# Performance work log

Measured on AMD Instinct MI355X. Metric: run time of the kernel, lower is better.

## Reference

```python
import jax, jax.numpy as jnp
import numpy as np

NUM_HEADS = 8
HEAD_DIM = 64
INPUT_DIM = 512
OUT_DIM = 512
INNER_DIM = NUM_HEADS * HEAD_DIM


def setup_inputs() -> dict:
    key = jax.random.key(0)
    ks = jax.random.split(key, 5)
    B, T = 4, 2048
    x = jax.random.normal(ks[0], (B, T, INPUT_DIM), dtype=jnp.float32)
    Wk = jax.random.normal(ks[1], (INNER_DIM, INPUT_DIM), dtype=jnp.float32)
    Wq = jax.random.normal(ks[2], (INNER_DIM, INPUT_DIM), dtype=jnp.float32)
    Wv = jax.random.normal(ks[3], (INNER_DIM, INPUT_DIM), dtype=jnp.float32)
    Wp = jax.random.normal(ks[4], (OUT_DIM, INNER_DIM), dtype=jnp.float32)
    return {"x": x, "Wk": Wk, "Wq": Wq, "Wv": Wv, "Wp": Wp, "causal_mask": 0}


def reference(x, Wk, Wq, Wv, Wp, causal_mask):
    B, T, C = x.shape
    c_scale = C ** (-0.5)

    def proj(W):
        # (B,T,C) @ (C,inner) -> (B,T,H,D) -> (B,H,T,D), scaled by C^-0.5
        return (jnp.einsum('btc,ic->bti', x, W)
                .reshape(B, T, NUM_HEADS, HEAD_DIM)
                .transpose(0, 2, 1, 3) * c_scale)

    q, k, v = proj(Wq), proj(Wk), proj(Wv)
    # scores: (B,H,T,T), scaled by head_dim^-0.5
    weight = jnp.einsum('bhqd,bhkd->bhqk', q, k) * (HEAD_DIM ** (-0.5))
    if causal_mask:
        mask = jnp.triu(jnp.ones((T, T), dtype=bool), k=1)
        weight = jnp.where(mask, -jnp.inf, weight)
    weight = jax.nn.softmax(weight, axis=-1)
    out = jnp.einsum('bhqk,bhkd->bhqd', weight, v)  # (B,H,T,D)
    out = out.transpose(0, 2, 1, 3).reshape(B, T, INNER_DIM)
    # final projection scaled by inner_dim^-0.5 (projection.size(-1))
    out = jnp.einsum('bti,oi->bto', out, Wp) * (INNER_DIM ** (-0.5))
    return out
```

## Files before the change

### kernel.cpp

```cpp
#include <hip/hip_runtime.h>
#include <stdint.h>

#define T_SEQ 2048
#define NB 4
#define NH 8
#define DH 64
#define CD 512

typedef __attribute__((ext_vector_type(8))) short bf16x8;
typedef __attribute__((ext_vector_type(4))) uint16_t u16x4;
typedef __attribute__((ext_vector_type(4))) float f32x4;
typedef __attribute__((ext_vector_type(16))) float f32x16;
typedef __attribute__((ext_vector_type(4))) int i32x4;

#if __has_builtin(__builtin_amdgcn_exp2f)
#define EXP2(x) __builtin_amdgcn_exp2f(x)
#else
#define EXP2(x) exp2f(x)
#endif

__device__ __forceinline__ uint16_t f2bf(float f) {
  uint32_t u = __float_as_uint(f);
  u += 0x7FFFu + ((u >> 16) & 1u);
  return (uint16_t)(u >> 16);
}

__device__ __forceinline__ uint32_t cvtpk_bf16(float lo, float hi) {
  uint32_t r;
  asm("v_cvt_pk_bf16_f32 %0, %1, %2" : "=v"(r) : "v"(lo), "v"(hi));
  return r;
}

__device__ __forceinline__ void gload_lds16(const void* g, void* l) {
  __builtin_amdgcn_global_load_lds((const __attribute__((address_space(1))) void*)g,
                                   (__attribute__((address_space(3))) void*)l, 16, 0, 0);
}

__global__ __launch_bounds__(256) void cvt_all(const float* __restrict__ x,
    const float* __restrict__ wq, const float* __restrict__ wk,
    const float* __restrict__ wv, const float* __restrict__ wp,
    uint16_t* __restrict__ ws) {
  int i = blockIdx.x * 256 + threadIdx.x;
  int e = i * 4;
  const float* src;
  uint16_t* dst;
  if (e < 4194304) {
    src = x + e; dst = ws + e;
  } else {
    int r = e - 4194304;
    int w = r >> 18;
    int o = r & 262143;
    const float* W = (w == 0) ? wq : (w == 1) ? wk : (w == 2) ? wv : wp;
    src = W + o;
    dst = ws + 4194304 + (w << 18) + o;
  }
  float4 v = *(const float4*)src;
  u16x4 o4 = { f2bf(v.x), f2bf(v.y), f2bf(v.z), f2bf(v.w) };
  *(u16x4*)dst = o4;
}

__device__ __forceinline__ void gemm_bt_tile(const uint16_t* __restrict__ A,
                                             const uint16_t* __restrict__ Bt,
                                             int m0, int n0,
                                             uint16_t* As, uint16_t* Bs,
                                             f32x4 acc[4][4]) {
  const int tid = threadIdx.x;
  const int lane = tid & 63;
  const int wave = tid >> 6;
  const int wr = (wave >> 1) * 64, wc = (wave & 1) * 64;
  const int l15 = lane & 15, l4 = lane >> 4;

#pragma unroll
  for (int m = 0; m < 4; ++m)
#pragma unroll
    for (int n = 0; n < 4; ++n)
      acc[m][n] = (f32x4){0.f, 0.f, 0.f, 0.f};

  for (int kt = 0; kt < 8; ++kt) {
#pragma unroll
    for (int is = 0; is < 4; ++is) {
      int p = is * 4096 + tid * 16;
      int g = p ^ (((p >> 7) & 7) << 4);
      int row = g >> 7, colb = g & 127;
      gload_lds16((const char*)A + (size_t)(m0 + row) * 1024 + kt * 128 + colb,
                  (char*)As + p);
      gload_lds16((const char*)Bt + (size_t)(n0 + row) * 1024 + kt * 128 + colb,
                  (char*)Bs + p);
    }
    __syncthreads();
#pragma unroll
    for (int ks = 0; ks < 2; ++ks) {
      bf16x8 af[4], bfr[4];
#pragma unroll
      for (int m = 0; m < 4; ++m) {
        int row = wr + m * 16 + l15;
        int byt = (row * 128 + ks * 64 + l4 * 16) ^ ((row & 7) << 4);
        af[m] = *(const bf16x8*)((const char*)As + byt);
      }
#pragma unroll
      for (int n = 0; n < 4; ++n) {
        int row = wc + n * 16 + l15;
        int byt = (row * 128 + ks * 64 + l4 * 16) ^ ((row & 7) << 4);
        bfr[n] = *(const bf16x8*)((const char*)Bs + byt);
      }
#pragma unroll
      for (int m = 0; m < 4; ++m)
#pragma unroll
        for (int n = 0; n < 4; ++n)
          acc[m][n] = __builtin_amdgcn_mfma_f32_16x16x32_bf16(af[m], bfr[n], acc[m][n], 0, 0, 0);
    }
    __syncthreads();
  }
}

__global__ __launch_bounds__(256) void proj_kernel(const uint16_t* __restrict__ xb,
    const uint16_t* __restrict__ wbase, uint16_t* __restrict__ qkv,
    float qscale, float kvscale) {
  __shared__ __align__(16) uint16_t As[128 * 64];
  __shared__ __align__(16) uint16_t Bs[128 * 64];
  int z = blockIdx.z;
  const uint16_t* W = wbase + (size_t)z * 262144;
  uint16_t* outb = qkv + (size_t)z * 4194304;
  float scale = (z == 0) ? qscale : kvscale;
  f32x4 acc[4][4];
  int lane = threadIdx.x & 63, wave = threadIdx.x >> 6;
  int wr = (wave >> 1) * 64, wc = (wave & 1) * 64;
  int l15 = lane & 15, l4 = lane >> 4;

  if (z < 2) {
    int m0 = blockIdx.x * 128, n0 = blockIdx.y * 128;
    gemm_bt_tile(xb, W, m0, n0, As, Bs, acc);
#pragma unroll
    for (int m = 0; m < 4; ++m)
#pragma unroll
      for (int n = 0; n < 4; ++n)
#pragma unroll
        for (int j = 0; j < 4; ++j) {
          int row = m0 + wr + m * 16 + l4 * 4 + j;
          int col = n0 + wc + n * 16 + l15;
          int b = row >> 11, t = row & 2047;
          int h = col >> 6, d = col & 63;
          outb[((size_t)(b * NH + h) * T_SEQ + t) * DH + d] = f2bf(acc[m][n][j] * scale);
        }
  } else {
    int m0 = blockIdx.y * 128, n0 = blockIdx.x * 128;
    gemm_bt_tile(W, xb, m0, n0, As, Bs, acc);
#pragma unroll
    for (int m = 0; m < 4; ++m)
#pragma unroll
      for (int n = 0; n < 4; ++n)
#pragma unroll
        for (int j = 0; j < 4; ++j) {
          int row = m0 + wr + m * 16 + l4 * 4 + j;
          int col = n0 + wc + n * 16 + l15;
          int h = row >> 6, d = row & 63;
          int b = col >> 11, t = col & 2047;
          outb[((size_t)(b * NH + h) * DH + d) * T_SEQ + t] = f2bf(acc[m][n][j] * scale);
        }
  }
}

__global__ __launch_bounds__(512, 4) void attn5(const uint16_t* __restrict__ Q,
    const uint16_t* __restrict__ K, const uint16_t* __restrict__ VT,
    uint16_t* __restrict__ AO) {
  __shared__ __align__(16) char smem[65536];

  int bid = blockIdx.x;
  int swz = (bid & 7) * 64 + (bid >> 3);
  int qt = swz & 15, bh = swz >> 4;
  int b = bh >> 3, h = bh & 7;
  int tid = threadIdx.x, lane = tid & 63, wave = tid >> 6;
  int l31 = lane & 31, hi = lane >> 5;
  int p = tid >> 8;
  int tin = tid & 255;
  int w4 = wave & 3;

  const char* Kb  = (const char*)(K  + (size_t)bh * T_SEQ * DH) + (size_t)p * 131072;
  const char* VTb = (const char*)(VT + (size_t)bh * DH * T_SEQ);
  const uint16_t* Qrow = Q + ((size_t)bh * T_SEQ + qt * 128 + w4 * 32 + l31) * DH;
  char* pbase = smem + p * 32768;

  auto stage = [&](int t) {
    char* kd = pbase + (t & 1) * 8192;
    char* vd = pbase + 16384 + (t & 1) * 8192;
    const char* ksrc = Kb + (size_t)t * 8192;
#pragma unroll
    for (int c = 0; c < 2; ++c) {
      int pp = c * 4096 + tin * 16;
      int g = pp ^ (((pp >> 7) & 7) << 4);
      gload_lds16(ksrc + g, kd + pp);
      int row = g >> 7, off = g & 127;
      gload_lds16(VTb + (size_t)row * 4096 + p * 2048 + (size_t)t * 128 + off, vd + pp);
    }
  };

  bf16x8 qf[4];
#pragma unroll
  for (int m = 0; m < 4; ++m)
    qf[m] = *(const bf16x8*)((const char*)Qrow + m * 32 + hi * 16);

  f32x16 Oacc[2];
#pragma unroll
  for (int dB = 0; dB < 2; ++dB) Oacc[dB] = (f32x16)(0.f);
  float lp0 = 0.f, lp1 = 0.f, lp2 = 0.f, lp3 = 0.f;

  stage(0);

  for (int kt = 0; kt < 16; ++kt) {
    if (kt + 1 < 16) stage(kt + 1);
    if (kt + 1 < 16) asm volatile("s_waitcnt vmcnt(4)\n\ts_barrier" ::: "memory");
    else             asm volatile("s_waitcnt vmcnt(0)\n\ts_barrier" ::: "memory");

    const char* Kc = pbase + (kt & 1) * 8192;
    const char* Vc = pbase + 16384 + (kt & 1) * 8192;

    f32x16 s0 = (f32x16)(0.f), s1 = (f32x16)(0.f);
    __builtin_amdgcn_s_setprio(1);
#pragma unroll
    for (int m = 0; m < 4; ++m) {
      int row0 = l31;
      int byt0 = (row0 * 128 + m * 32 + hi * 16) ^ ((row0 & 7) << 4);
      bf16x8 kf0 = *(const bf16x8*)(Kc + byt0);
      s0 = __builtin_amdgcn_mfma_f32_32x32x16_bf16(kf0, qf[m], s0, 0, 0, 0);
      int row1 = 32 + l31;
      int byt1 = (row1 * 128 + m * 32 + hi * 16) ^ ((row1 & 7) << 4);
      bf16x8 kf1 = *(const bf16x8*)(Kc + byt1);
      s1 = __builtin_amdgcn_mfma_f32_32x32x16_bf16(kf1, qf[m], s1, 0, 0, 0);
    }
    __builtin_amdgcn_s_setprio(0);

    uint32_t pa_[2][4], pb_[2][4];
    {
      float e0[16], e1[16];
#pragma unroll
      for (int r = 0; r < 16; ++r) e0[r] = EXP2(s0[r]);
#pragma unroll
      for (int r = 0; r < 16; ++r) e1[r] = EXP2(s1[r]);
#pragma unroll
      for (int r = 0; r < 16; ++r) {
        if ((r & 3) == 0)      { lp0 += e0[r]; lp0 += e1[r]; }
        else if ((r & 3) == 1) { lp1 += e0[r]; lp1 += e1[r]; }
        else if ((r & 3) == 2) { lp2 += e0[r]; lp2 += e1[r]; }
        else                   { lp3 += e0[r]; lp3 += e1[r]; }
      }
#pragma unroll
      for (int g = 0; g < 4; ++g) {
        pa_[0][g] = cvtpk_bf16(e0[4 * g], e0[4 * g + 1]);
        pb_[0][g] = cvtpk_bf16(e0[4 * g + 2], e0[4 * g + 3]);
        pa_[1][g] = cvtpk_bf16(e1[4 * g], e1[4 * g + 1]);
        pb_[1][g] = cvtpk_bf16(e1[4 * g + 2], e1[4 * g + 3]);
      }
    }

#pragma unroll
    for (int km = 0; km < 4; ++km) {
      const int Tt = km >> 1;
      const int g0 = (km & 1) * 2;
      uint32_t w0 = pa_[Tt][g0], w2 = pa_[Tt][g0 + 1];
      uint32_t w1 = pb_[Tt][g0], w3 = pb_[Tt][g0 + 1];
      asm volatile("v_permlane32_swap_b32 %0, %1" : "+v"(w0), "+v"(w2));
      asm volatile("v_permlane32_swap_b32 %0, %1" : "+v"(w1), "+v"(w3));
      i32x4 pw = { (int)w0, (int)w1, (int)w2, (int)w3 };
      bf16x8 paf = __builtin_bit_cast(bf16x8, pw);
      __builtin_amdgcn_s_setprio(1);
#pragma unroll
      for (int dB = 0; dB < 2; ++dB) {
        int row = dB * 32 + l31;
        int byt = (row * 128 + km * 32 + hi * 16) ^ ((row & 7) << 4);
        bf16x8 vf = *(const bf16x8*)(Vc + byt);
        Oacc[dB] = __builtin_amdgcn_mfma_f32_32x32x16_bf16(paf, vf, Oacc[dB], 0, 0, 0);
      }
      __builtin_amdgcn_s_setprio(0);
    }

    asm volatile("s_waitcnt lgkmcnt(0)\n\ts_barrier" ::: "memory");
  }

  float lpart = (lp0 + lp1) + (lp2 + lp3);
  float lsum = lpart + __shfl_xor(lpart, 32, 64);
  float* cm = (float*)smem;
  float* slot = cm + (size_t)w4 * 2112 + lane * 33;
  if (p == 1) {
#pragma unroll
    for (int dB = 0; dB < 2; ++dB)
#pragma unroll
      for (int r = 0; r < 16; ++r)
        slot[dB * 16 + r] = Oacc[dB][r];
    slot[32] = lsum;
  }
  __syncthreads();
  if (p == 0) {
    float inv = 1.f / (lsum + slot[32]);
    f32x16 o0, o1;
#pragma unroll
    for (int r = 0; r < 16; ++r) {
      o0[r] = Oacc[0][r] + slot[r];
      o1[r] = Oacc[1][r] + slot[16 + r];
    }
    int qb0 = qt * 128 + w4 * 32;
#pragma unroll
    for (int r = 0; r < 16; ++r) {
      int qoff = (r & 3) + 8 * (r >> 2) + 4 * hi;
      float invr = __shfl(inv, qoff, 64);
      int t = qb0 + qoff;
      size_t base = ((size_t)(b * T_SEQ + t)) * 512 + h * 64;
      AO[base + l31]      = f2bf(o0[r] * invr);
      AO[base + 32 + l31] = f2bf(o1[r] * invr);
    }
  }
}

__global__ __launch_bounds__(256) void final_kernel(const uint16_t* __restrict__ ab,
    const uint16_t* __restrict__ wpb, float* __restrict__ out, float scale) {
  __shared__ __align__(16) uint16_t As[128 * 64];
  __shared__ __align__(16) uint16_t Bs[128 * 64];
  int m0 = blockIdx.x * 128, n0 = blockIdx.y * 128;
  f32x4 acc[4][4];
  gemm_bt_tile(ab, wpb, m0, n0, As, Bs, acc);
  int lane = threadIdx.x & 63, wave = threadIdx.x >> 6;
  int wr = (wave >> 1) * 64, wc = (wave & 1) * 64;
  int l15 = lane & 15, l4 = lane >> 4;
#pragma unroll
  for (int m = 0; m < 4; ++m)
#pragma unroll
    for (int n = 0; n < 4; ++n)
#pragma unroll
      for (int j = 0; j < 4; ++j) {
        int row = m0 + wr + m * 16 + l4 * 4 + j;
        int col = n0 + wc + n * 16 + l15;
        out[(size_t)row * 512 + col] = acc[m][n][j] * scale;
      }
}

extern "C" void kernel_launch(void* const* d_in, const int* in_sizes, int n_in,
                              void* d_out, int out_size, void* d_ws, size_t ws_size,
                              hipStream_t stream) {
  const float* x  = (const float*)d_in[0];
  const float* Wk = (const float*)d_in[1];
  const float* Wq = (const float*)d_in[2];
  const float* Wv = (const float*)d_in[3];
  const float* Wp = (const float*)d_in[4];
  uint16_t* ws = (uint16_t*)d_ws;

  uint16_t* xb  = ws;
  uint16_t* wqb = ws + 4194304;
  uint16_t* qkv = ws + 4194304 + 4 * 262144;
  uint16_t* qb  = qkv;
  uint16_t* kb  = qkv + 4194304;
  uint16_t* vtb = qkv + 2 * 4194304;
  uint16_t* ao  = xb;
  uint16_t* wpb = wqb + 3 * 262144;

  const float c_scale = 0.04419417382415922f;
  const float qscale = c_scale * 0.125f * 1.4426950408889634f;
  const float fscale = c_scale;

  cvt_all<<<dim3(5120), dim3(256), 0, stream>>>(x, Wq, Wk, Wv, Wp, ws);
  proj_kernel<<<dim3(64, 4, 3), dim3(256), 0, stream>>>(xb, wqb, qkv, qscale, c_scale);
  attn5<<<dim3(512), dim3(512), 0, stream>>>(qb, kb, vtb, ao);
  final_kernel<<<dim3(64, 4), dim3(256), 0, stream>>>(ao, wpb, (float*)d_out, fscale);
}
```

Baseline: 91.25 us.

## Split attention over four key ranges with a separate combine kernel

Adds an attention kernel that divides the key sequence into four chunks. Each of 2048 smaller blocks computes unnormalized partial outputs and row sums for one chunk, and a new combine kernel adds the partials, normalizes them and writes the head-interleaved layout. This raises the number of independent blocks, and the V operand is now read straight from global memory instead of being staged in LDS. In exchange it writes and re-reads bf16 partial outputs through workspace, adds a kernel launch, and only takes this path when the workspace is large enough.

```diff
diff --git a/kernel.cpp b/kernel.cpp
--- a/kernel.cpp
+++ b/kernel.cpp
@@ -8,6 +8,7 @@
 #define CD 512
 
 typedef __attribute__((ext_vector_type(8))) short bf16x8;
+typedef __attribute__((ext_vector_type(8))) uint16_t u16x8;
 typedef __attribute__((ext_vector_type(4))) uint16_t u16x4;
 typedef __attribute__((ext_vector_type(4))) float f32x4;
 typedef __attribute__((ext_vector_type(16))) float f32x16;
@@ -23,6 +24,10 @@
   uint32_t u = __float_as_uint(f);
   u += 0x7FFFu + ((u >> 16) & 1u);
   return (uint16_t)(u >> 16);
+}
+
+__device__ __forceinline__ float bf2f(uint16_t u) {
+  return __uint_as_float(((uint32_t)u) << 16);
 }
 
 __device__ __forceinline__ uint32_t cvtpk_bf16(float lo, float hi) {
@@ -160,6 +165,143 @@
   }
 }
 
+__global__ __launch_bounds__(256) void attn6(const uint16_t* __restrict__ Q,
+    const uint16_t* __restrict__ K, const uint16_t* __restrict__ VT,
+    uint16_t* __restrict__ Op, float* __restrict__ Lp) {
+  __shared__ __align__(16) char kbuf[2][8192];
+
+  int bid = blockIdx.x;
+  int swz = (bid & 7) * 256 + (bid >> 3);
+  int qt = swz & 15, qtr = (swz >> 4) & 3, bh = swz >> 6;
+  int tid = threadIdx.x, lane = tid & 63, wave = tid >> 6;
+  int l31 = lane & 31, hi = lane >> 5;
+
+  const char* Kb = (const char*)(K + (size_t)bh * T_SEQ * DH) + (size_t)qtr * 65536;
+  const char* Vb = (const char*)(VT + (size_t)bh * DH * T_SEQ) + (size_t)qtr * 1024
+                   + (size_t)l31 * 4096 + (size_t)hi * 16;
+  const uint16_t* Qrow = Q + ((size_t)bh * T_SEQ + qt * 128 + wave * 32 + l31) * DH;
+
+  auto stage = [&](int t) {
+    char* kd = &kbuf[t & 1][0];
+    const char* ksrc = Kb + (size_t)t * 8192;
+#pragma unroll
+    for (int c = 0; c < 2; ++c) {
+      int pp = c * 4096 + tid * 16;
+      int g = pp ^ (((pp >> 7) & 7) << 4);
+      gload_lds16(ksrc + g, kd + pp);
+    }
+  };
+
+  bf16x8 qf[4];
+#pragma unroll
+  for (int m = 0; m < 4; ++m)
+    qf[m] = *(const bf16x8*)((const char*)Qrow + m * 32 + hi * 16);
+
+  f32x16 Oacc[2];
+  Oacc[0] = (f32x16)(0.f);
+  Oacc[1] = (f32x16)(0.f);
+  float lp0 = 0.f, lp1 = 0.f, lp2 = 0.f, lp3 = 0.f;
+
+  stage(0);
+  asm volatile("s_waitcnt vmcnt(0)\n\ts_barrier" ::: "memory");
+
+  for (int kt = 0; kt < 8; ++kt) {
+    if (kt + 1 < 8) stage(kt + 1);
+    const char* Kc = &kbuf[kt & 1][0];
+
+    f32x16 s0 = (f32x16)(0.f), s1 = (f32x16)(0.f);
+    __builtin_amdgcn_s_setprio(1);
+#pragma unroll
+    for (int m = 0; m < 4; ++m) {
+      int byt0 = (l31 * 128 + m * 32 + hi * 16) ^ ((l31 & 7) << 4);
+      bf16x8 kf0 = *(const bf16x8*)(Kc + byt0);
+      s0 = __builtin_amdgcn_mfma_f32_32x32x16_bf16(kf0, qf[m], s0, 0, 0, 0);
+      int row1 = 32 + l31;
+      int byt1 = (row1 * 128 + m * 32 + hi * 16) ^ ((row1 & 7) << 4);
+      bf16x8 kf1 = *(const bf16x8*)(Kc + byt1);
+      s1 = __builtin_amdgcn_mfma_f32_32x32x16_bf16(kf1, qf[m], s1, 0, 0, 0);
+    }
+    __builtin_amdgcn_s_setprio(0);
+
+    uint32_t pa_[2][4], pb_[2][4];
+    {
+      float e0[16], e1[16];
+#pragma unroll
+      for (int r = 0; r < 16; ++r) e0[r] = EXP2(s0[r]);
+#pragma unroll
+      for (int r = 0; r < 16; ++r) e1[r] = EXP2(s1[r]);
+#pragma unroll
+      for (int r = 0; r < 16; ++r) {
+        if ((r & 3) == 0)      { lp0 += e0[r]; lp0 += e1[r]; }
+        else if ((r & 3) == 1) { lp1 += e0[r]; lp1 += e1[r]; }
+        else if ((r & 3) == 2) { lp2 += e0[r]; lp2 += e1[r]; }
+        else                   { lp3 += e0[r]; lp3 += e1[r]; }
+      }
+#pragma unroll
+      for (int g = 0; g < 4; ++g) {
+        pa_[0][g] = cvtpk_bf16(e0[4 * g], e0[4 * g + 1]);
+        pb_[0][g] = cvtpk_bf16(e0[4 * g + 2], e0[4 * g + 3]);
+        pa_[1][g] = cvtpk_bf16(e1[4 * g], e1[4 * g + 1]);
+        pb_[1][g] = cvtpk_bf16(e1[4 * g + 2], e1[4 * g + 3]);
+      }
+    }
+
+    const char* Vs = Vb + (size_t)kt * 128;
+#pragma unroll
+    for (int km = 0; km < 4; ++km) {
+      const int Tt = km >> 1;
+      const int g0 = (km & 1) * 2;
+      uint32_t w0 = pa_[Tt][g0], w2 = pa_[Tt][g0 + 1];
+      uint32_t w1 = pb_[Tt][g0], w3 = pb_[Tt][g0 + 1];
+      asm volatile("v_permlane32_swap_b32 %0, %1" : "+v"(w0), "+v"(w2));
+      asm volatile("v_permlane32_swap_b32 %0, %1" : "+v"(w1), "+v"(w3));
+      i32x4 pw = { (int)w0, (int)w1, (int)w2, (int)w3 };
+      bf16x8 paf = __builtin_bit_cast(bf16x8, pw);
+      bf16x8 vf0 = *(const bf16x8*)(Vs + km * 32);
+      bf16x8 vf1 = *(const bf16x8*)(Vs + km * 32 + 131072);
+      __builtin_amdgcn_s_setprio(1);
+      Oacc[0] = __builtin_amdgcn_mfma_f32_32x32x16_bf16(paf, vf0, Oacc[0], 0, 0, 0);
+      Oacc[1] = __builtin_amdgcn_mfma_f32_32x32x16_bf16(paf, vf1, Oacc[1], 0, 0, 0);
+      __builtin_amdgcn_s_setprio(0);
+    }
+
+    if (kt + 1 < 8) asm volatile("s_waitcnt vmcnt(0)\n\ts_barrier" ::: "memory");
+  }
+
+  float lpart = (lp0 + lp1) + (lp2 + lp3);
+  float lsum = lpart + __shfl_xor(lpart, 32, 64);
+  int rowbase = bh * 2048 + qt * 128 + wave * 32;
+  if (hi == 0) Lp[qtr * 65536 + rowbase + l31] = lsum;
+  uint16_t* Oq = Op + (size_t)qtr * 65536 * 64;
+#pragma unroll
+  for (int r = 0; r < 16; ++r) {
+    int qoff = (r & 3) + 8 * (r >> 2) + 4 * hi;
+    size_t ro = (size_t)(rowbase + qoff);
+    Oq[ro * 64 + l31]      = f2bf(Oacc[0][r]);
+    Oq[ro * 64 + 32 + l31] = f2bf(Oacc[1][r]);
+  }
+}
+
+__global__ __launch_bounds__(256) void combine4(const uint16_t* __restrict__ Op,
+    const float* __restrict__ Lp, uint16_t* __restrict__ ao) {
+  int idx = blockIdx.x * 256 + threadIdx.x;
+  int row = idx >> 3, d0 = (idx & 7) * 8;
+  float inv = 1.f / (Lp[row] + Lp[65536 + row] + Lp[131072 + row] + Lp[196608 + row]);
+  float acc[8] = {0.f, 0.f, 0.f, 0.f, 0.f, 0.f, 0.f, 0.f};
+#pragma unroll
+  for (int q = 0; q < 4; ++q) {
+    u16x8 v = *(const u16x8*)(Op + ((size_t)q * 65536 + row) * 64 + d0);
+#pragma unroll
+    for (int j = 0; j < 8; ++j) acc[j] += bf2f(v[j]);
+  }
+  int bh = row >> 11, t = row & 2047;
+  int b = bh >> 3, h = bh & 7;
+  u16x8 o;
+#pragma unroll
+  for (int j = 0; j < 8; ++j) o[j] = f2bf(acc[j] * inv);
+  *(u16x8*)(ao + ((size_t)(b * 2048 + t) * 512 + h * 64 + d0)) = o;
+}
+
 __global__ __launch_bounds__(512, 4) void attn5(const uint16_t* __restrict__ Q,
     const uint16_t* __restrict__ K, const uint16_t* __restrict__ VT,
     uint16_t* __restrict__ AO) {
@@ -200,8 +342,8 @@
     qf[m] = *(const bf16x8*)((const char*)Qrow + m * 32 + hi * 16);
 
   f32x16 Oacc[2];
-#pragma unroll
-  for (int dB = 0; dB < 2; ++dB) Oacc[dB] = (f32x16)(0.f);
+  Oacc[0] = (f32x16)(0.f);
+  Oacc[1] = (f32x16)(0.f);
   float lp0 = 0.f, lp1 = 0.f, lp2 = 0.f, lp3 = 0.f;
 
   stage(0);
@@ -218,8 +360,7 @@
     __builtin_amdgcn_s_setprio(1);
 #pragma unroll
     for (int m = 0; m < 4; ++m) {
-      int row0 = l31;
-      int byt0 = (row0 * 128 + m * 32 + hi * 16) ^ ((row0 & 7) << 4);
+      int byt0 = (l31 * 128 + m * 32 + hi * 16) ^ ((l31 & 7) << 4);
       bf16x8 kf0 = *(const bf16x8*)(Kc + byt0);
       s0 = __builtin_amdgcn_mfma_f32_32x32x16_bf16(kf0, qf[m], s0, 0, 0, 0);
       int row1 = 32 + l31;
@@ -351,12 +492,21 @@
   uint16_t* ao  = xb;
   uint16_t* wpb = wqb + 3 * 262144;
 
+  uint16_t* opart = ws + 17825792;
+  float*    lpart = (float*)(ws + 34603008);
+  const bool big_ws = (ws_size >= 70254592ull);
+
   const float c_scale = 0.04419417382415922f;
   const float qscale = c_scale * 0.125f * 1.4426950408889634f;
   const float fscale = c_scale;
 
   cvt_all<<<dim3(5120), dim3(256), 0, stream>>>(x, Wq, Wk, Wv, Wp, ws);
   proj_kernel<<<dim3(64, 4, 3), dim3(256), 0, stream>>>(xb, wqb, qkv, qscale, c_scale);
-  attn5<<<dim3(512), dim3(512), 0, stream>>>(qb, kb, vtb, ao);
+  if (big_ws) {
+    attn6<<<dim3(2048), dim3(256), 0, stream>>>(qb, kb, vtb, opart, lpart);
+    combine4<<<dim3(2048), dim3(256), 0, stream>>>(opart, lpart, ao);
+  } else {
+    attn5<<<dim3(512), dim3(512), 0, stream>>>(qb, kb, vtb, ao);
+  }
   final_kernel<<<dim3(64, 4), dim3(256), 0, stream>>>(ao, wpb, (float*)d_out, fscale);
 }
```

New measurement: 133.6 us. 46.4% more time.

## Load V fragments directly into registers and deepen K LDS ring to four buffers

Applied to the files above, without the earlier changes.

The attention kernel stops staging V tiles through shared memory. Each wave now reads its V^T fragments straight from global memory into registers at the top of every key tile. K is still staged through LDS, but in a four-slot ring with a prefetch distance of two tiles, and a single vmcnt-based barrier per iteration. This frees LDS bandwidth and gives memory loads more time to land before use, at the cost of redundant global/L2 reads of V across the four waves sharing a head and higher register pressure.

```diff
diff --git a/kernel.cpp b/kernel.cpp
--- a/kernel.cpp
+++ b/kernel.cpp
@@ -160,7 +160,7 @@
   }
 }
 
-__global__ __launch_bounds__(512, 4) void attn5(const uint16_t* __restrict__ Q,
+__global__ __launch_bounds__(512, 4) void attn7(const uint16_t* __restrict__ Q,
     const uint16_t* __restrict__ K, const uint16_t* __restrict__ VT,
     uint16_t* __restrict__ AO) {
   __shared__ __align__(16) char smem[65536];
@@ -175,22 +175,21 @@
   int tin = tid & 255;
   int w4 = wave & 3;
 
-  const char* Kb  = (const char*)(K  + (size_t)bh * T_SEQ * DH) + (size_t)p * 131072;
-  const char* VTb = (const char*)(VT + (size_t)bh * DH * T_SEQ);
+  const char* Kb = (const char*)(K + (size_t)bh * T_SEQ * DH) + (size_t)p * 131072;
+  const char* Vb0 = (const char*)(VT + (size_t)bh * DH * T_SEQ)
+                    + (size_t)l31 * 4096 + (size_t)p * 2048 + (size_t)hi * 16;
+  const char* Vb1 = Vb0 + (size_t)32 * 4096;
   const uint16_t* Qrow = Q + ((size_t)bh * T_SEQ + qt * 128 + w4 * 32 + l31) * DH;
   char* pbase = smem + p * 32768;
 
-  auto stage = [&](int t) {
-    char* kd = pbase + (t & 1) * 8192;
-    char* vd = pbase + 16384 + (t & 1) * 8192;
+  auto stageK = [&](int t) {
+    char* kd = pbase + (t & 3) * 8192;
     const char* ksrc = Kb + (size_t)t * 8192;
 #pragma unroll
     for (int c = 0; c < 2; ++c) {
       int pp = c * 4096 + tin * 16;
       int g = pp ^ (((pp >> 7) & 7) << 4);
       gload_lds16(ksrc + g, kd + pp);
-      int row = g >> 7, off = g & 127;
-      gload_lds16(VTb + (size_t)row * 4096 + p * 2048 + (size_t)t * 128 + off, vd + pp);
     }
   };
 
@@ -200,26 +199,32 @@
     qf[m] = *(const bf16x8*)((const char*)Qrow + m * 32 + hi * 16);
 
   f32x16 Oacc[2];
-#pragma unroll
-  for (int dB = 0; dB < 2; ++dB) Oacc[dB] = (f32x16)(0.f);
+  Oacc[0] = (f32x16)(0.f);
+  Oacc[1] = (f32x16)(0.f);
   float lp0 = 0.f, lp1 = 0.f, lp2 = 0.f, lp3 = 0.f;
 
-  stage(0);
+  stageK(0);
+  stageK(1);
+  asm volatile("s_waitcnt vmcnt(2)\n\ts_barrier" ::: "memory");
 
   for (int kt = 0; kt < 16; ++kt) {
-    if (kt + 1 < 16) stage(kt + 1);
-    if (kt + 1 < 16) asm volatile("s_waitcnt vmcnt(4)\n\ts_barrier" ::: "memory");
-    else             asm volatile("s_waitcnt vmcnt(0)\n\ts_barrier" ::: "memory");
-
-    const char* Kc = pbase + (kt & 1) * 8192;
-    const char* Vc = pbase + 16384 + (kt & 1) * 8192;
+    const char* vs0 = Vb0 + (size_t)kt * 128;
+    const char* vs1 = Vb1 + (size_t)kt * 128;
+    bf16x8 vreg[8];
+#pragma unroll
+    for (int km = 0; km < 4; ++km) {
+      vreg[2 * km]     = *(const bf16x8*)(vs0 + km * 32);
+      vreg[2 * km + 1] = *(const bf16x8*)(vs1 + km * 32);
+    }
+    if (kt + 2 < 16) stageK(kt + 2);
+
+    const char* Kc = pbase + (kt & 3) * 8192;
 
     f32x16 s0 = (f32x16)(0.f), s1 = (f32x16)(0.f);
     __builtin_amdgcn_s_setprio(1);
 #pragma unroll
     for (int m = 0; m < 4; ++m) {
-      int row0 = l31;
-      int byt0 = (row0 * 128 + m * 32 + hi * 16) ^ ((row0 & 7) << 4);
+      int byt0 = (l31 * 128 + m * 32 + hi * 16) ^ ((l31 & 7) << 4);
       bf16x8 kf0 = *(const bf16x8*)(Kc + byt0);
       s0 = __builtin_amdgcn_mfma_f32_32x32x16_bf16(kf0, qf[m], s0, 0, 0, 0);
       int row1 = 32 + l31;
@@ -258,22 +263,17 @@
       const int g0 = (km & 1) * 2;
       uint32_t w0 = pa_[Tt][g0], w2 = pa_[Tt][g0 + 1];
       uint32_t w1 = pb_[Tt][g0], w3 = pb_[Tt][g0 + 1];
-      asm volatile("v_permlane32_swap_b32 %0, %1" : "+v"(w0), "+v"(w2));
-      asm volatile("v_permlane32_swap_b32 %0, %1" : "+v"(w1), "+v"(w3));
+      asm("v_permlane32_swap_b32 %0, %1" : "+v"(w0), "+v"(w2));
+      asm("v_permlane32_swap_b32 %0, %1" : "+v"(w1), "+v"(w3));
       i32x4 pw = { (int)w0, (int)w1, (int)w2, (int)w3 };
       bf16x8 paf = __builtin_bit_cast(bf16x8, pw);
       __builtin_amdgcn_s_setprio(1);
-#pragma unroll
-      for (int dB = 0; dB < 2; ++dB) {
-        int row = dB * 32 + l31;
-        int byt = (row * 128 + km * 32 + hi * 16) ^ ((row & 7) << 4);
-        bf16x8 vf = *(const bf16x8*)(Vc + byt);
-        Oacc[dB] = __builtin_amdgcn_mfma_f32_32x32x16_bf16(paf, vf, Oacc[dB], 0, 0, 0);
-      }
+      Oacc[0] = __builtin_amdgcn_mfma_f32_32x32x16_bf16(paf, vreg[2 * km],     Oacc[0], 0, 0, 0);
+      Oacc[1] = __builtin_amdgcn_mfma_f32_32x32x16_bf16(paf, vreg[2 * km + 1], Oacc[1], 0, 0, 0);
       __builtin_amdgcn_s_setprio(0);
     }
 
-    asm volatile("s_waitcnt lgkmcnt(0)\n\ts_barrier" ::: "memory");
+    asm volatile("s_waitcnt vmcnt(2)\n\ts_barrier" ::: "memory");
   }
 
   float lpart = (lp0 + lp1) + (lp2 + lp3);
@@ -357,6 +357,6 @@
 
   cvt_all<<<dim3(5120), dim3(256), 0, stream>>>(x, Wq, Wk, Wv, Wp, ws);
   proj_kernel<<<dim3(64, 4, 3), dim3(256), 0, stream>>>(xb, wqb, qkv, qscale, c_scale);
-  attn5<<<dim3(512), dim3(512), 0, stream>>>(qb, kb, vtb, ao);
+  attn7<<<dim3(512), dim3(512), 0, stream>>>(qb, kb, vtb, ao);
   final_kernel<<<dim3(64, 4), dim3(256), 0, stream>>>(ao, wpb, (float*)d_out, fscale);
 }
```

Result: slower. 169.8 us (+86.0%).

## Split attention key range across four wave groups with 1024-thread blocks

Applied to the files above, without the earlier changes.

The attention kernel now runs 1024 threads per block, with four partitions of 256 threads each handling a quarter of the key sequence instead of two halves. Each partition processes 32-key tiles per step, and the K/V staging switches to an unswizzled per-lane layout in LDS. Partial outputs and row sums are combined through shared memory in two passes. The aim is more parallelism per query tile to hide latency, at the cost of extra reduction work, barriers, and possible LDS bank conflicts from dropping the XOR swizzle.

```diff
diff --git a/kernel.cpp b/kernel.cpp
--- a/kernel.cpp
+++ b/kernel.cpp
@@ -160,7 +160,7 @@
   }
 }
 
-__global__ __launch_bounds__(512, 4) void attn5(const uint16_t* __restrict__ Q,
+__global__ __launch_bounds__(1024, 8) void attn9(const uint16_t* __restrict__ Q,
     const uint16_t* __restrict__ K, const uint16_t* __restrict__ VT,
     uint16_t* __restrict__ AO) {
   __shared__ __align__(16) char smem[65536];
@@ -169,29 +169,23 @@
   int swz = (bid & 7) * 64 + (bid >> 3);
   int qt = swz & 15, bh = swz >> 4;
   int b = bh >> 3, h = bh & 7;
-  int tid = threadIdx.x, lane = tid & 63, wave = tid >> 6;
+  int tid = threadIdx.x, lane = tid & 63;
   int l31 = lane & 31, hi = lane >> 5;
   int p = tid >> 8;
   int tin = tid & 255;
-  int w4 = wave & 3;
-
-  const char* Kb  = (const char*)(K  + (size_t)bh * T_SEQ * DH) + (size_t)p * 131072;
-  const char* VTb = (const char*)(VT + (size_t)bh * DH * T_SEQ);
+  int w4 = (tid >> 6) & 3;
+
+  const char* Kb  = (const char*)(K + (size_t)bh * T_SEQ * DH) + (size_t)p * 65536;
+  const char* VTb = (const char*)(VT + (size_t)bh * DH * T_SEQ) + (size_t)p * 1024;
   const uint16_t* Qrow = Q + ((size_t)bh * T_SEQ + qt * 128 + w4 * 32 + l31) * DH;
-  char* pbase = smem + p * 32768;
+  char* pb = smem + p * 16384;
 
   auto stage = [&](int t) {
-    char* kd = pbase + (t & 1) * 8192;
-    char* vd = pbase + 16384 + (t & 1) * 8192;
-    const char* ksrc = Kb + (size_t)t * 8192;
-#pragma unroll
-    for (int c = 0; c < 2; ++c) {
-      int pp = c * 4096 + tin * 16;
-      int g = pp ^ (((pp >> 7) & 7) << 4);
-      gload_lds16(ksrc + g, kd + pp);
-      int row = g >> 7, off = g & 127;
-      gload_lds16(VTb + (size_t)row * 4096 + p * 2048 + (size_t)t * 128 + off, vd + pp);
-    }
+    char* kd = pb + (t & 1) * 4096;
+    char* vd = pb + 8192 + (t & 1) * 4096;
+    gload_lds16(Kb + (size_t)(t * 32 + l31) * 128 + w4 * 32 + hi * 16, kd + tin * 16);
+    gload_lds16(VTb + (size_t)lane * 4096 + t * 64 + (w4 >> 1) * 32 + (w4 & 1) * 16,
+                vd + tin * 16);
   };
 
   bf16x8 qf[4];
@@ -200,76 +194,61 @@
     qf[m] = *(const bf16x8*)((const char*)Qrow + m * 32 + hi * 16);
 
   f32x16 Oacc[2];
-#pragma unroll
-  for (int dB = 0; dB < 2; ++dB) Oacc[dB] = (f32x16)(0.f);
+  Oacc[0] = (f32x16)(0.f);
+  Oacc[1] = (f32x16)(0.f);
   float lp0 = 0.f, lp1 = 0.f, lp2 = 0.f, lp3 = 0.f;
 
   stage(0);
 
   for (int kt = 0; kt < 16; ++kt) {
     if (kt + 1 < 16) stage(kt + 1);
-    if (kt + 1 < 16) asm volatile("s_waitcnt vmcnt(4)\n\ts_barrier" ::: "memory");
+    if (kt + 1 < 16) asm volatile("s_waitcnt vmcnt(2)\n\ts_barrier" ::: "memory");
     else             asm volatile("s_waitcnt vmcnt(0)\n\ts_barrier" ::: "memory");
 
-    const char* Kc = pbase + (kt & 1) * 8192;
-    const char* Vc = pbase + 16384 + (kt & 1) * 8192;
-
-    f32x16 s0 = (f32x16)(0.f), s1 = (f32x16)(0.f);
+    const char* Kc = pb + (kt & 1) * 4096;
+    const char* Vc = pb + 8192 + (kt & 1) * 4096;
+
+    f32x16 s = (f32x16)(0.f);
     __builtin_amdgcn_s_setprio(1);
 #pragma unroll
     for (int m = 0; m < 4; ++m) {
-      int row0 = l31;
-      int byt0 = (row0 * 128 + m * 32 + hi * 16) ^ ((row0 & 7) << 4);
-      bf16x8 kf0 = *(const bf16x8*)(Kc + byt0);
-      s0 = __builtin_amdgcn_mfma_f32_32x32x16_bf16(kf0, qf[m], s0, 0, 0, 0);
-      int row1 = 32 + l31;
-      int byt1 = (row1 * 128 + m * 32 + hi * 16) ^ ((row1 & 7) << 4);
-      bf16x8 kf1 = *(const bf16x8*)(Kc + byt1);
-      s1 = __builtin_amdgcn_mfma_f32_32x32x16_bf16(kf1, qf[m], s1, 0, 0, 0);
+      bf16x8 kf = *(const bf16x8*)(Kc + m * 1024 + hi * 512 + l31 * 16);
+      s = __builtin_amdgcn_mfma_f32_32x32x16_bf16(kf, qf[m], s, 0, 0, 0);
     }
     __builtin_amdgcn_s_setprio(0);
 
-    uint32_t pa_[2][4], pb_[2][4];
+    uint32_t pa_[4], pb_[4];
     {
-      float e0[16], e1[16];
-#pragma unroll
-      for (int r = 0; r < 16; ++r) e0[r] = EXP2(s0[r]);
-#pragma unroll
-      for (int r = 0; r < 16; ++r) e1[r] = EXP2(s1[r]);
+      float e[16];
+#pragma unroll
+      for (int r = 0; r < 16; ++r) e[r] = EXP2(s[r]);
 #pragma unroll
       for (int r = 0; r < 16; ++r) {
-        if ((r & 3) == 0)      { lp0 += e0[r]; lp0 += e1[r]; }
-        else if ((r & 3) == 1) { lp1 += e0[r]; lp1 += e1[r]; }
-        else if ((r & 3) == 2) { lp2 += e0[r]; lp2 += e1[r]; }
-        else                   { lp3 += e0[r]; lp3 += e1[r]; }
+        if ((r & 3) == 0)      lp0 += e[r];
+        else if ((r & 3) == 1) lp1 += e[r];
+        else if ((r & 3) == 2) lp2 += e[r];
+        else                   lp3 += e[r];
       }
 #pragma unroll
       for (int g = 0; g < 4; ++g) {
-        pa_[0][g] = cvtpk_bf16(e0[4 * g], e0[4 * g + 1]);
-        pb_[0][g] = cvtpk_bf16(e0[4 * g + 2], e0[4 * g + 3]);
-        pa_[1][g] = cvtpk_bf16(e1[4 * g], e1[4 * g + 1]);
-        pb_[1][g] = cvtpk_bf16(e1[4 * g + 2], e1[4 * g + 3]);
-      }
-    }
-
-#pragma unroll
-    for (int km = 0; km < 4; ++km) {
-      const int Tt = km >> 1;
-      const int g0 = (km & 1) * 2;
-      uint32_t w0 = pa_[Tt][g0], w2 = pa_[Tt][g0 + 1];
-      uint32_t w1 = pb_[Tt][g0], w3 = pb_[Tt][g0 + 1];
-      asm volatile("v_permlane32_swap_b32 %0, %1" : "+v"(w0), "+v"(w2));
-      asm volatile("v_permlane32_swap_b32 %0, %1" : "+v"(w1), "+v"(w3));
+        pa_[g] = cvtpk_bf16(e[4 * g], e[4 * g + 1]);
+        pb_[g] = cvtpk_bf16(e[4 * g + 2], e[4 * g + 3]);
+      }
+    }
+
+#pragma unroll
+    for (int km = 0; km < 2; ++km) {
+      uint32_t w0 = pa_[2 * km], w2 = pa_[2 * km + 1];
+      uint32_t w1 = pb_[2 * km], w3 = pb_[2 * km + 1];
+      asm("v_permlane32_swap_b32 %0, %1" : "+v"(w0), "+v"(w2));
+      asm("v_permlane32_swap_b32 %0, %1" : "+v"(w1), "+v"(w3));
       i32x4 pw = { (int)w0, (int)w1, (int)w2, (int)w3 };
       bf16x8 paf = __builtin_bit_cast(bf16x8, pw);
+      bf16x8 vf0 = *(const bf16x8*)(Vc + km * 2048 + hi * 1024 + l31 * 16);
+      bf16x8 vf1 = *(const bf16x8*)(Vc + km * 2048 + hi * 1024 + 512 + l31 * 16);
       __builtin_amdgcn_s_setprio(1);
-#pragma unroll
-      for (int dB = 0; dB < 2; ++dB) {
-        int row = dB * 32 + l31;
-        int byt = (row * 128 + km * 32 + hi * 16) ^ ((row & 7) << 4);
-        bf16x8 vf = *(const bf16x8*)(Vc + byt);
-        Oacc[dB] = __builtin_amdgcn_mfma_f32_32x32x16_bf16(paf, vf, Oacc[dB], 0, 0, 0);
-      }
+      Oacc[0] = __builtin_amdgcn_mfma_f32_32x32x16_bf16(paf, vf0, Oacc[0], 0, 0, 0);
+      Oacc[1] = __builtin_amdgcn_mfma_f32_32x32x16_bf16(paf, vf1, Oacc[1], 0, 0, 0);
       __builtin_amdgcn_s_setprio(0);
     }
 
@@ -278,24 +257,42 @@
 
   float lpart = (lp0 + lp1) + (lp2 + lp3);
   float lsum = lpart + __shfl_xor(lpart, 32, 64);
-  float* cm = (float*)smem;
-  float* slot = cm + (size_t)w4 * 2112 + lane * 33;
-  if (p == 1) {
-#pragma unroll
-    for (int dB = 0; dB < 2; ++dB)
-#pragma unroll
-      for (int r = 0; r < 16; ++r)
-        slot[dB * 16 + r] = Oacc[dB][r];
-    slot[32] = lsum;
+  float* slab = (float*)smem;
+  int sidx = ((p - 1) * 256 + tin) * 17;
+
+  if (p) {
+#pragma unroll
+    for (int r = 0; r < 16; ++r) slab[sidx + r] = Oacc[0][r];
+    slab[sidx + 16] = lsum;
   }
   __syncthreads();
-  if (p == 0) {
-    float inv = 1.f / (lsum + slot[32]);
-    f32x16 o0, o1;
-#pragma unroll
-    for (int r = 0; r < 16; ++r) {
-      o0[r] = Oacc[0][r] + slot[r];
-      o1[r] = Oacc[1][r] + slot[16 + r];
+  float inv = 0.f;
+  f32x16 o0;
+  if (!p) {
+    float lt = lsum;
+    o0 = Oacc[0];
+#pragma unroll
+    for (int pp = 0; pp < 3; ++pp) {
+      int si = (pp * 256 + tin) * 17;
+#pragma unroll
+      for (int r = 0; r < 16; ++r) o0[r] += slab[si + r];
+      lt += slab[si + 16];
+    }
+    inv = 1.f / lt;
+  }
+  __syncthreads();
+  if (p) {
+#pragma unroll
+    for (int r = 0; r < 16; ++r) slab[sidx + r] = Oacc[1][r];
+  }
+  __syncthreads();
+  if (!p) {
+    f32x16 o1 = Oacc[1];
+#pragma unroll
+    for (int pp = 0; pp < 3; ++pp) {
+      int si = (pp * 256 + tin) * 17;
+#pragma unroll
+      for (int r = 0; r < 16; ++r) o1[r] += slab[si + r];
     }
     int qb0 = qt * 128 + w4 * 32;
 #pragma unroll
@@ -357,6 +354,6 @@
 
   cvt_all<<<dim3(5120), dim3(256), 0, stream>>>(x, Wq, Wk, Wv, Wp, ws);
   proj_kernel<<<dim3(64, 4, 3), dim3(256), 0, stream>>>(xb, wqb, qkv, qscale, c_scale);
-  attn5<<<dim3(512), dim3(512), 0, stream>>>(qb, kb, vtb, ao);
+  attn9<<<dim3(512), dim3(1024), 0, stream>>>(qb, kb, vtb, ao);
   final_kernel<<<dim3(64, 4), dim3(256), 0, stream>>>(ao, wpb, (float*)d_out, fscale);
 }
```

Result: slower. 170.7 us (+87.1%).
